# Kernel tuning notes

Measured on AMD Instinct MI355X. Metric: run time of the kernel, lower is better.

Reference implementation:

```python
import jax, jax.numpy as jnp
import numpy as np

H = 2048        # hidden_size
NH = 16         # num q heads
NKV = 4         # num kv heads
HD = 128        # head_dim
G = NH // NKV   # GQA group size
B = 32          # batch (decode sequences)
S = 4096        # max kv cache length per sequence
SCALE = HD ** -0.5
NEG = -1e30


def setup_inputs() -> dict:
    key = jax.random.key(0)
    ks = jax.random.split(key, 6)
    hidden_states = jax.random.normal(ks[0], (B, 1, H), dtype=jnp.float32)
    kv_cache = jax.random.normal(ks[1], (B, S, 2, NKV, HD), dtype=jnp.float32)
    seq_lens = jax.random.randint(ks[2], (B,), 1, S, dtype=jnp.int32)
    slot_mapping = seq_lens - 1  # write current token's k/v at its slot
    positions = (seq_lens - 1)[:, None].astype(jnp.int32)
    Wqkv = jax.random.normal(ks[3], (H, (NH + 2 * NKV) * HD), dtype=jnp.float32) * (H ** -0.5)
    bqkv = jax.random.normal(ks[4], ((NH + 2 * NKV) * HD,), dtype=jnp.float32) * 0.02
    Wo = jax.random.normal(ks[5], (NH * HD, H), dtype=jnp.float32) * ((NH * HD) ** -0.5)
    return {"hidden_states": hidden_states, "positions": positions, "kv_cache": kv_cache,
            "slot_mapping": slot_mapping, "seq_lens": seq_lens,
            "Wqkv": Wqkv, "bqkv": bqkv, "Wo": Wo}


def reference(hidden_states, positions, kv_cache, slot_mapping, seq_lens, Wqkv, bqkv, Wo):
    b, t, _ = hidden_states.shape  # t == 1 (decode)
    qkv = hidden_states.reshape(b * t, H) @ Wqkv + bqkv          # [B, (NH+2NKV)*HD]
    q, k, v = jnp.split(qkv, [NH * HD, (NH + NKV) * HD], axis=-1)
    q = q.reshape(b, NKV, G, HD)                                  # grouped-query layout
    k = k.reshape(b, NKV, HD)
    v = v.reshape(b, NKV, HD)
    # scatter current-step k/v into the paged cache at slot_mapping
    rows = jnp.arange(b)
    cache = kv_cache.at[rows, slot_mapping, 0].set(k)
    cache = cache.at[rows, slot_mapping, 1].set(v)
    keys = cache[:, :, 0]   # [B, S, NKV, HD]
    vals = cache[:, :, 1]   # [B, S, NKV, HD]
    # attention scores with ragged seq_lens mask
    scores = jnp.einsum('bkgd,bskd->bkgs', q, keys) * SCALE       # [B, NKV, G, S]
    valid = (jnp.arange(S)[None, :] < seq_lens[:, None])          # [B, S]
    scores = jnp.where(valid[:, None, None, :], scores, NEG)
    probs = jax.nn.softmax(scores, axis=-1)
    out = jnp.einsum('bkgs,bskd->bkgd', probs, vals)              # [B, NKV, G, HD]
    out = out.reshape(b * t, NH * HD)
    return (out @ Wo).reshape(b, t, H)
```

## Files before the change

kernel.cpp:

```cpp
#include <hip/hip_runtime.h>
#include <cstddef>

#define HQ 2048
#define NKVH 4
#define HDIM 128
#define QKV_N 3072
#define ATT_SCALE 0.08838834764831845f
#define KSPLIT 16
#define CHUNK 128
#define NCH 32

__device__ __forceinline__ float4 f4max(float4 a, float4 b) {
  return make_float4(fmaxf(a.x, b.x), fmaxf(a.y, b.y), fmaxf(a.z, b.z), fmaxf(a.w, b.w));
}

template <int N>
__global__ __launch_bounds__(256) void proj_kernel(const float* __restrict__ X,
                                                   const float* __restrict__ W,
                                                   float* __restrict__ part) {
  __shared__ union {
    float x[32][128];
    float red[32][4][64];
  } sm;
  const int t = threadIdx.x;
  const int c0 = blockIdx.x << 6;
  const int ksb = blockIdx.y;
  const int k0 = ksb << 7;
  const int c = t & 63;
  const int ksub = t >> 6;

#pragma unroll
  for (int i = 0; i < 4; ++i) {
    const int id = t + (i << 8);
    const int bb = id >> 5, kk = (id & 31) << 2;
    *reinterpret_cast<float4*>(&sm.x[bb][kk]) =
        *reinterpret_cast<const float4*>(X + bb * HQ + k0 + kk);
  }
  __syncthreads();

  float acc[32];
#pragma unroll
  for (int b = 0; b < 32; ++b) acc[b] = 0.f;

#pragma unroll
  for (int kk4 = 0; kk4 < 8; ++kk4) {
    const int kk = (ksub << 5) + (kk4 << 2);
    const float* wp = W + (size_t)(k0 + kk) * N + c0 + c;
    const float w0 = wp[0];
    const float w1 = wp[N];
    const float w2 = wp[2 * N];
    const float w3 = wp[3 * N];
#pragma unroll
    for (int b = 0; b < 32; ++b) {
      const float4 x4 = *reinterpret_cast<const float4*>(&sm.x[b][kk]);
      acc[b] = fmaf(x4.x, w0, acc[b]);
      acc[b] = fmaf(x4.y, w1, acc[b]);
      acc[b] = fmaf(x4.z, w2, acc[b]);
      acc[b] = fmaf(x4.w, w3, acc[b]);
    }
  }
  __syncthreads();
#pragma unroll
  for (int b = 0; b < 32; ++b) sm.red[b][ksub][c] = acc[b];
  __syncthreads();
#pragma unroll
  for (int i = 0; i < 8; ++i) {
    const int o = t + (i << 8);
    const int b = o >> 6, cc = o & 63;
    const float v = sm.red[b][0][cc] + sm.red[b][1][cc] + sm.red[b][2][cc] + sm.red[b][3][cc];
    part[(size_t)(ksb * 32 + b) * N + c0 + cc] = v;
  }
}

template <int NCOL, bool HAS_BIAS>
__global__ __launch_bounds__(256) void reduce_kernel(const float* __restrict__ part,
                                                     const float* __restrict__ bias,
                                                     float* __restrict__ out) {
  const int o = blockIdx.x * 256 + threadIdx.x;
  constexpr int total = 32 * NCOL;
  float s = 0.f;
#pragma unroll
  for (int ks = 0; ks < KSPLIT; ++ks) s += part[(size_t)ks * total + o];
  if (HAS_BIAS) s += bias[o % NCOL];
  out[o] = s;
}

__global__ __launch_bounds__(256) void attn_kernel(const float* __restrict__ cache,
                                                   const int* __restrict__ seq_lens,
                                                   const int* __restrict__ slot_map,
                                                   const float* __restrict__ qkv,
                                                   float* __restrict__ ml,
                                                   float* __restrict__ accp) {
  __shared__ float pt[CHUNK][4];
  __shared__ float pvbuf[4][128][4];
  __shared__ float redm[4][4];
  __shared__ float redl[4][4];

  const int t = threadIdx.x;
  const int bid = blockIdx.x;
  const int chunk = bid & 31;
  const int kvh = (bid >> 5) & 3;
  const int b = bid >> 7;
  const int L = seq_lens[b];
  const int start = chunk << 7;
  if (start >= L) return;
  const int n = min(CHUNK, L - start);
  const int send = start + n;
  const int slot = slot_map[b];
  const float* __restrict__ qrow = qkv + b * QKV_N;
  const float* __restrict__ knew = qrow + 2048 + (kvh << 7);
  const float* __restrict__ vnew = qrow + 2560 + (kvh << 7);

  const int w = t >> 6, l = t & 63;
  const int l16 = l & 15, rq = l >> 4;
  const int wbase = w << 5;

  float4 qr[4][2];
#pragma unroll
  for (int g = 0; g < 4; ++g) {
#pragma unroll
    for (int e = 0; e < 2; ++e)
      qr[g][e] = *reinterpret_cast<const float4*>(qrow + ((kvh << 2) + g) * HDIM +
                                                  (l16 << 3) + (e << 2));
  }

  auto krow_ptr = [&](int r) -> const float* {
    int sg = start + r;
    sg = (sg < send) ? sg : start;
    return (sg == slot) ? knew : cache + (((size_t)((b << 12) + sg)) << 10) + (kvh << 7);
  };
  auto vrow_ptr = [&](int r) -> const float* {
    int sg = start + r;
    sg = (sg < send) ? sg : start;
    return (sg == slot) ? vnew : cache + (((size_t)((b << 12) + sg)) << 10) + 512 + (kvh << 7);
  };

  auto kload = [&](int st, float4* dst) {
#pragma unroll
    for (int rg = 0; rg < 4; ++rg) {
      const float* kp = krow_ptr(wbase + (st << 4) + (rg << 2) + rq) + (l16 << 3);
      dst[2 * rg] = *reinterpret_cast<const float4*>(kp);
      dst[2 * rg + 1] = *reinterpret_cast<const float4*>(kp + 4);
    }
  };
  auto vload = [&](int vt, float2* dst) {
#pragma unroll
    for (int s = 0; s < 16; ++s)
      dst[s] = *reinterpret_cast<const float2*>(vrow_ptr(wbase + (vt << 4) + s) + (l << 1));
  };

  float4 m4 = make_float4(-1e30f, -1e30f, -1e30f, -1e30f);
  auto score_st = [&](int st, const float4* kr) {
#pragma unroll
    for (int rg = 0; rg < 4; ++rg) {
      const float4 k0 = kr[2 * rg], k1 = kr[2 * rg + 1];
      float s0 = fmaf(k0.x, qr[0][0].x, fmaf(k0.y, qr[0][0].y, fmaf(k0.z, qr[0][0].z, k0.w * qr[0][0].w)));
      s0 = fmaf(k1.x, qr[0][1].x, fmaf(k1.y, qr[0][1].y, fmaf(k1.z, qr[0][1].z, fmaf(k1.w, qr[0][1].w, s0))));
      float s1 = fmaf(k0.x, qr[1][0].x, fmaf(k0.y, qr[1][0].y, fmaf(k0.z, qr[1][0].z, k0.w * qr[1][0].w)));
      s1 = fmaf(k1.x, qr[1][1].x, fmaf(k1.y, qr[1][1].y, fmaf(k1.z, qr[1][1].z, fmaf(k1.w, qr[1][1].w, s1))));
      float s2 = fmaf(k0.x, qr[2][0].x, fmaf(k0.y, qr[2][0].y, fmaf(k0.z, qr[2][0].z, k0.w * qr[2][0].w)));
      s2 = fmaf(k1.x, qr[2][1].x, fmaf(k1.y, qr[2][1].y, fmaf(k1.z, qr[2][1].z, fmaf(k1.w, qr[2][1].w, s2))));
      float s3 = fmaf(k0.x, qr[3][0].x, fmaf(k0.y, qr[3][0].y, fmaf(k0.z, qr[3][0].z, k0.w * qr[3][0].w)));
      s3 = fmaf(k1.x, qr[3][1].x, fmaf(k1.y, qr[3][1].y, fmaf(k1.z, qr[3][1].z, fmaf(k1.w, qr[3][1].w, s3))));
#pragma unroll
      for (int off = 1; off <= 8; off <<= 1) {
        s0 += __shfl_xor(s0, off);
        s1 += __shfl_xor(s1, off);
        s2 += __shfl_xor(s2, off);
        s3 += __shfl_xor(s3, off);
      }
      const int row = wbase + (st << 4) + (rg << 2) + rq;
      const float4 sc = make_float4(s0 * ATT_SCALE, s1 * ATT_SCALE, s2 * ATT_SCALE, s3 * ATT_SCALE);
      if (row < n) m4 = f4max(m4, sc);
      if (l16 == 0) *reinterpret_cast<float4*>(&pt[row][0]) = sc;
    }
  };

  float4 ka[8];
  float2 va[16], vb[16];
  kload(0, ka);
  vload(0, va);
  score_st(0, ka);
  kload(1, ka);
  score_st(1, ka);

  m4.x = fmaxf(m4.x, __shfl_xor(m4.x, 16));
  m4.y = fmaxf(m4.y, __shfl_xor(m4.y, 16));
  m4.z = fmaxf(m4.z, __shfl_xor(m4.z, 16));
  m4.w = fmaxf(m4.w, __shfl_xor(m4.w, 16));
  m4.x = fmaxf(m4.x, __shfl_xor(m4.x, 32));
  m4.y = fmaxf(m4.y, __shfl_xor(m4.y, 32));
  m4.z = fmaxf(m4.z, __shfl_xor(m4.z, 32));
  m4.w = fmaxf(m4.w, __shfl_xor(m4.w, 32));
  if (l == 0) *reinterpret_cast<float4*>(&redm[w][0]) = m4;
  __syncthreads();
  float4 M4 = *reinterpret_cast<const float4*>(&redm[0][0]);
  M4 = f4max(M4, *reinterpret_cast<const float4*>(&redm[1][0]));
  M4 = f4max(M4, *reinterpret_cast<const float4*>(&redm[2][0]));
  M4 = f4max(M4, *reinterpret_cast<const float4*>(&redm[3][0]));

  vload(1, vb);

  float4 l4 = make_float4(0.f, 0.f, 0.f, 0.f);
  if (l < 32) {
    const int r = wbase + l;
    float4 e = make_float4(0.f, 0.f, 0.f, 0.f);
    if (r < n) {
      const float4 v = *reinterpret_cast<const float4*>(&pt[r][0]);
      e.x = __expf(v.x - M4.x);
      e.y = __expf(v.y - M4.y);
      e.z = __expf(v.z - M4.z);
      e.w = __expf(v.w - M4.w);
    }
    *reinterpret_cast<float4*>(&pt[r][0]) = e;
    l4 = e;
  }
#pragma unroll
  for (int off = 1; off <= 32; off <<= 1) {
    l4.x += __shfl_xor(l4.x, off);
    l4.y += __shfl_xor(l4.y, off);
    l4.z += __shfl_xor(l4.z, off);
    l4.w += __shfl_xor(l4.w, off);
  }
  if (l == 0) *reinterpret_cast<float4*>(&redl[w][0]) = l4;

  float4 accA = make_float4(0.f, 0.f, 0.f, 0.f);
  float4 accB = make_float4(0.f, 0.f, 0.f, 0.f);
#pragma unroll
  for (int s = 0; s < 16; ++s) {
    const float4 p = *reinterpret_cast<const float4*>(&pt[wbase + s][0]);
    const float2 vv = va[s];
    accA.x = fmaf(p.x, vv.x, accA.x); accA.y = fmaf(p.y, vv.x, accA.y);
    accA.z = fmaf(p.z, vv.x, accA.z); accA.w = fmaf(p.w, vv.x, accA.w);
    accB.x = fmaf(p.x, vv.y, accB.x); accB.y = fmaf(p.y, vv.y, accB.y);
    accB.z = fmaf(p.z, vv.y, accB.z); accB.w = fmaf(p.w, vv.y, accB.w);
  }
#pragma unroll
  for (int s = 0; s < 16; ++s) {
    const float4 p = *reinterpret_cast<const float4*>(&pt[wbase + 16 + s][0]);
    const float2 vv = vb[s];
    accA.x = fmaf(p.x, vv.x, accA.x); accA.y = fmaf(p.y, vv.x, accA.y);
    accA.z = fmaf(p.z, vv.x, accA.z); accA.w = fmaf(p.w, vv.x, accA.w);
    accB.x = fmaf(p.x, vv.y, accB.x); accB.y = fmaf(p.y, vv.y, accB.y);
    accB.z = fmaf(p.z, vv.y, accB.z); accB.w = fmaf(p.w, vv.y, accB.w);
  }

  *reinterpret_cast<float4*>(&pvbuf[w][l << 1][0]) = accA;
  *reinterpret_cast<float4*>(&pvbuf[w][(l << 1) + 1][0]) = accB;
  __syncthreads();

  if (t < 128) {
    const int d = t;
    float4 s0 = *reinterpret_cast<const float4*>(&pvbuf[0][d][0]);
    const float4 s1 = *reinterpret_cast<const float4*>(&pvbuf[1][d][0]);
    const float4 s2 = *reinterpret_cast<const float4*>(&pvbuf[2][d][0]);
    const float4 s3 = *reinterpret_cast<const float4*>(&pvbuf[3][d][0]);
    s0.x += s1.x + s2.x + s3.x;
    s0.y += s1.y + s2.y + s3.y;
    s0.z += s1.z + s2.z + s3.z;
    s0.w += s1.w + s2.w + s3.w;
    float* ap = accp + (size_t)bid * 512;
    ap[d] = s0.x;
    ap[128 + d] = s0.y;
    ap[256 + d] = s0.z;
    ap[384 + d] = s0.w;
  }
  if (t == 0) {
    float4 Lt = *reinterpret_cast<const float4*>(&redl[0][0]);
    const float4 l1 = *reinterpret_cast<const float4*>(&redl[1][0]);
    const float4 l2 = *reinterpret_cast<const float4*>(&redl[2][0]);
    const float4 l3 = *reinterpret_cast<const float4*>(&redl[3][0]);
    Lt.x += l1.x + l2.x + l3.x;
    Lt.y += l1.y + l2.y + l3.y;
    Lt.z += l1.z + l2.z + l3.z;
    Lt.w += l1.w + l2.w + l3.w;
    *reinterpret_cast<float4*>(ml + (size_t)bid * 8) = M4;
    *reinterpret_cast<float4*>(ml + (size_t)bid * 8 + 4) = Lt;
  }
}

__global__ __launch_bounds__(128) void combine_kernel(const int* __restrict__ seq_lens,
                                                      const float* __restrict__ ml,
                                                      const float* __restrict__ accp,
                                                      float* __restrict__ attn) {
  const int blk = blockIdx.x;
  const int g = blk & 3, kvh = (blk >> 2) & 3, b = blk >> 4;
  const int d = threadIdx.x;
  const int L = seq_lens[b];
  const int nch = (L + CHUNK - 1) >> 7;
  const int base = (b * 4 + kvh) * NCH;

  float M = -1e30f;
  for (int c = 0; c < nch; ++c) M = fmaxf(M, ml[(size_t)(base + c) * 8 + g]);
  float osum = 0.f, lsum = 0.f;
  for (int c = 0; c < nch; ++c) {
    const int idx = base + c;
    const float mc = ml[(size_t)idx * 8 + g];
    const float lc = ml[(size_t)idx * 8 + 4 + g];
    const float wgt = __expf(mc - M);
    lsum = fmaf(lc, wgt, lsum);
    osum = fmaf(wgt, accp[(size_t)idx * 512 + g * 128 + d], osum);
  }
  attn[(size_t)b * HQ + kvh * 512 + g * 128 + d] = osum / lsum;
}

extern "C" void kernel_launch(void* const* d_in, const int* in_sizes, int n_in,
                              void* d_out, int out_size, void* d_ws, size_t ws_size,
                              hipStream_t stream) {
  const float* hidden = (const float*)d_in[0];
  const float* cache = (const float*)d_in[2];
  const int* slot_map = (const int*)d_in[3];
  const int* seq_lens = (const int*)d_in[4];
  const float* Wqkv = (const float*)d_in[5];
  const float* bqkv = (const float*)d_in[6];
  const float* Wo = (const float*)d_in[7];
  float* out = (float*)d_out;
  float* ws = (float*)d_ws;

  float* qkv_part = ws;
  float* qkv      = ws + 1572864;
  float* ml       = ws + 1671168;
  float* accp     = ws + 1703936;
  float* attn     = ws + 3801088;
  float* o_part   = ws + 3866624;

  proj_kernel<QKV_N><<<dim3(48, KSPLIT), 256, 0, stream>>>(hidden, Wqkv, qkv_part);
  reduce_kernel<QKV_N, true><<<384, 256, 0, stream>>>(qkv_part, bqkv, qkv);
  attn_kernel<<<4096, 256, 0, stream>>>(cache, seq_lens, slot_map, qkv, ml, accp);
  combine_kernel<<<512, 128, 0, stream>>>(seq_lens, ml, accp, attn);
  proj_kernel<HQ><<<dim3(32, KSPLIT), 256, 0, stream>>>(attn, Wo, o_part);
  reduce_kernel<HQ, false><<<256, 256, 0, stream>>>(o_part, nullptr, out);
}
```

Measured before the change: 125.0 us.

## Halve attention chunk size to 64 rows and keep scores in registers

Split the KV sequence into 64-row chunks instead of 128, doubling the attention grid so more blocks can keep memory requests in flight. Each wave now handles 16 rows, so scores stay in registers and the softmax exponentials are computed in place, which removes the shared-memory round trip for raw scores. A launch-bounds occupancy hint is added. The cost is more partial results for the combine kernel to read and more per-block overhead for short sequences.

```diff
diff --git a/kernel.cpp b/kernel.cpp
--- a/kernel.cpp
+++ b/kernel.cpp
@@ -7,8 +7,8 @@
 #define QKV_N 3072
 #define ATT_SCALE 0.08838834764831845f
 #define KSPLIT 16
-#define CHUNK 128
-#define NCH 32
+#define CHUNK 64
+#define NCH 64
 
 __device__ __forceinline__ float4 f4max(float4 a, float4 b) {
   return make_float4(fmaxf(a.x, b.x), fmaxf(a.y, b.y), fmaxf(a.z, b.z), fmaxf(a.w, b.w));
@@ -85,24 +85,24 @@
   out[o] = s;
 }
 
-__global__ __launch_bounds__(256) void attn_kernel(const float* __restrict__ cache,
-                                                   const int* __restrict__ seq_lens,
-                                                   const int* __restrict__ slot_map,
-                                                   const float* __restrict__ qkv,
-                                                   float* __restrict__ ml,
-                                                   float* __restrict__ accp) {
-  __shared__ float pt[CHUNK][4];
+__global__ __launch_bounds__(256, 4) void attn_kernel(const float* __restrict__ cache,
+                                                      const int* __restrict__ seq_lens,
+                                                      const int* __restrict__ slot_map,
+                                                      const float* __restrict__ qkv,
+                                                      float* __restrict__ ml,
+                                                      float* __restrict__ accp) {
+  __shared__ float pt[4][16][4];
   __shared__ float pvbuf[4][128][4];
   __shared__ float redm[4][4];
   __shared__ float redl[4][4];
 
   const int t = threadIdx.x;
   const int bid = blockIdx.x;
-  const int chunk = bid & 31;
-  const int kvh = (bid >> 5) & 3;
-  const int b = bid >> 7;
+  const int chunk = bid & 63;
+  const int kvh = (bid >> 6) & 3;
+  const int b = bid >> 8;
   const int L = seq_lens[b];
-  const int start = chunk << 7;
+  const int start = chunk << 6;
   if (start >= L) return;
   const int n = min(CHUNK, L - start);
   const int send = start + n;
@@ -113,16 +113,7 @@
 
   const int w = t >> 6, l = t & 63;
   const int l16 = l & 15, rq = l >> 4;
-  const int wbase = w << 5;
-
-  float4 qr[4][2];
-#pragma unroll
-  for (int g = 0; g < 4; ++g) {
-#pragma unroll
-    for (int e = 0; e < 2; ++e)
-      qr[g][e] = *reinterpret_cast<const float4*>(qrow + ((kvh << 2) + g) * HDIM +
-                                                  (l16 << 3) + (e << 2));
-  }
+  const int wbase = w << 4;
 
   auto krow_ptr = [&](int r) -> const float* {
     int sg = start + r;
@@ -135,54 +126,49 @@
     return (sg == slot) ? vnew : cache + (((size_t)((b << 12) + sg)) << 10) + 512 + (kvh << 7);
   };
 
-  auto kload = [&](int st, float4* dst) {
-#pragma unroll
-    for (int rg = 0; rg < 4; ++rg) {
-      const float* kp = krow_ptr(wbase + (st << 4) + (rg << 2) + rq) + (l16 << 3);
-      dst[2 * rg] = *reinterpret_cast<const float4*>(kp);
-      dst[2 * rg + 1] = *reinterpret_cast<const float4*>(kp + 4);
+  float4 qr[4][2];
+#pragma unroll
+  for (int g = 0; g < 4; ++g) {
+#pragma unroll
+    for (int e = 0; e < 2; ++e)
+      qr[g][e] = *reinterpret_cast<const float4*>(qrow + ((kvh << 2) + g) * HDIM +
+                                                  (l16 << 3) + (e << 2));
+  }
+  float4 ka[8];
+#pragma unroll
+  for (int rg = 0; rg < 4; ++rg) {
+    const float* kp = krow_ptr(wbase + (rg << 2) + rq) + (l16 << 3);
+    ka[2 * rg] = *reinterpret_cast<const float4*>(kp);
+    ka[2 * rg + 1] = *reinterpret_cast<const float4*>(kp + 4);
+  }
+  float2 va[16];
+#pragma unroll
+  for (int s = 0; s < 16; ++s)
+    va[s] = *reinterpret_cast<const float2*>(vrow_ptr(wbase + s) + (l << 1));
+
+  float4 m4 = make_float4(-1e30f, -1e30f, -1e30f, -1e30f);
+  float4 scr[4];
+#pragma unroll
+  for (int rg = 0; rg < 4; ++rg) {
+    const float4 k0 = ka[2 * rg], k1 = ka[2 * rg + 1];
+    float s0 = fmaf(k0.x, qr[0][0].x, fmaf(k0.y, qr[0][0].y, fmaf(k0.z, qr[0][0].z, k0.w * qr[0][0].w)));
+    s0 = fmaf(k1.x, qr[0][1].x, fmaf(k1.y, qr[0][1].y, fmaf(k1.z, qr[0][1].z, fmaf(k1.w, qr[0][1].w, s0))));
+    float s1 = fmaf(k0.x, qr[1][0].x, fmaf(k0.y, qr[1][0].y, fmaf(k0.z, qr[1][0].z, k0.w * qr[1][0].w)));
+    s1 = fmaf(k1.x, qr[1][1].x, fmaf(k1.y, qr[1][1].y, fmaf(k1.z, qr[1][1].z, fmaf(k1.w, qr[1][1].w, s1))));
+    float s2 = fmaf(k0.x, qr[2][0].x, fmaf(k0.y, qr[2][0].y, fmaf(k0.z, qr[2][0].z, k0.w * qr[2][0].w)));
+    s2 = fmaf(k1.x, qr[2][1].x, fmaf(k1.y, qr[2][1].y, fmaf(k1.z, qr[2][1].z, fmaf(k1.w, qr[2][1].w, s2))));
+    float s3 = fmaf(k0.x, qr[3][0].x, fmaf(k0.y, qr[3][0].y, fmaf(k0.z, qr[3][0].z, k0.w * qr[3][0].w)));
+    s3 = fmaf(k1.x, qr[3][1].x, fmaf(k1.y, qr[3][1].y, fmaf(k1.z, qr[3][1].z, fmaf(k1.w, qr[3][1].w, s3))));
+#pragma unroll
+    for (int off = 1; off <= 8; off <<= 1) {
+      s0 += __shfl_xor(s0, off);
+      s1 += __shfl_xor(s1, off);
+      s2 += __shfl_xor(s2, off);
+      s3 += __shfl_xor(s3, off);
     }
-  };
-  auto vload = [&](int vt, float2* dst) {
-#pragma unroll
-    for (int s = 0; s < 16; ++s)
-      dst[s] = *reinterpret_cast<const float2*>(vrow_ptr(wbase + (vt << 4) + s) + (l << 1));
-  };
-
-  float4 m4 = make_float4(-1e30f, -1e30f, -1e30f, -1e30f);
-  auto score_st = [&](int st, const float4* kr) {
-#pragma unroll
-    for (int rg = 0; rg < 4; ++rg) {
-      const float4 k0 = kr[2 * rg], k1 = kr[2 * rg + 1];
-      float s0 = fmaf(k0.x, qr[0][0].x, fmaf(k0.y, qr[0][0].y, fmaf(k0.z, qr[0][0].z, k0.w * qr[0][0].w)));
-      s0 = fmaf(k1.x, qr[0][1].x, fmaf(k1.y, qr[0][1].y, fmaf(k1.z, qr[0][1].z, fmaf(k1.w, qr[0][1].w, s0))));
-      float s1 = fmaf(k0.x, qr[1][0].x, fmaf(k0.y, qr[1][0].y, fmaf(k0.z, qr[1][0].z, k0.w * qr[1][0].w)));
-      s1 = fmaf(k1.x, qr[1][1].x, fmaf(k1.y, qr[1][1].y, fmaf(k1.z, qr[1][1].z, fmaf(k1.w, qr[1][1].w, s1))));
-      float s2 = fmaf(k0.x, qr[2][0].x, fmaf(k0.y, qr[2][0].y, fmaf(k0.z, qr[2][0].z, k0.w * qr[2][0].w)));
-      s2 = fmaf(k1.x, qr[2][1].x, fmaf(k1.y, qr[2][1].y, fmaf(k1.z, qr[2][1].z, fmaf(k1.w, qr[2][1].w, s2))));
-      float s3 = fmaf(k0.x, qr[3][0].x, fmaf(k0.y, qr[3][0].y, fmaf(k0.z, qr[3][0].z, k0.w * qr[3][0].w)));
-      s3 = fmaf(k1.x, qr[3][1].x, fmaf(k1.y, qr[3][1].y, fmaf(k1.z, qr[3][1].z, fmaf(k1.w, qr[3][1].w, s3))));
-#pragma unroll
-      for (int off = 1; off <= 8; off <<= 1) {
-        s0 += __shfl_xor(s0, off);
-        s1 += __shfl_xor(s1, off);
-        s2 += __shfl_xor(s2, off);
-        s3 += __shfl_xor(s3, off);
-      }
-      const int row = wbase + (st << 4) + (rg << 2) + rq;
-      const float4 sc = make_float4(s0 * ATT_SCALE, s1 * ATT_SCALE, s2 * ATT_SCALE, s3 * ATT_SCALE);
-      if (row < n) m4 = f4max(m4, sc);
-      if (l16 == 0) *reinterpret_cast<float4*>(&pt[row][0]) = sc;
-    }
-  };
-
-  float4 ka[8];
-  float2 va[16], vb[16];
-  kload(0, ka);
-  vload(0, va);
-  score_st(0, ka);
-  kload(1, ka);
-  score_st(1, ka);
+    scr[rg] = make_float4(s0 * ATT_SCALE, s1 * ATT_SCALE, s2 * ATT_SCALE, s3 * ATT_SCALE);
+    if (wbase + (rg << 2) + rq < n) m4 = f4max(m4, scr[rg]);
+  }
 
   m4.x = fmaxf(m4.x, __shfl_xor(m4.x, 16));
   m4.y = fmaxf(m4.y, __shfl_xor(m4.y, 16));
@@ -199,46 +185,33 @@
   M4 = f4max(M4, *reinterpret_cast<const float4*>(&redm[2][0]));
   M4 = f4max(M4, *reinterpret_cast<const float4*>(&redm[3][0]));
 
-  vload(1, vb);
-
-  float4 l4 = make_float4(0.f, 0.f, 0.f, 0.f);
-  if (l < 32) {
-    const int r = wbase + l;
+  float4 lsum = make_float4(0.f, 0.f, 0.f, 0.f);
+#pragma unroll
+  for (int rg = 0; rg < 4; ++rg) {
+    const int row = wbase + (rg << 2) + rq;
     float4 e = make_float4(0.f, 0.f, 0.f, 0.f);
-    if (r < n) {
-      const float4 v = *reinterpret_cast<const float4*>(&pt[r][0]);
-      e.x = __expf(v.x - M4.x);
-      e.y = __expf(v.y - M4.y);
-      e.z = __expf(v.z - M4.z);
-      e.w = __expf(v.w - M4.w);
+    if (row < n) {
+      e.x = __expf(scr[rg].x - M4.x);
+      e.y = __expf(scr[rg].y - M4.y);
+      e.z = __expf(scr[rg].z - M4.z);
+      e.w = __expf(scr[rg].w - M4.w);
     }
-    *reinterpret_cast<float4*>(&pt[r][0]) = e;
-    l4 = e;
-  }
-#pragma unroll
-  for (int off = 1; off <= 32; off <<= 1) {
-    l4.x += __shfl_xor(l4.x, off);
-    l4.y += __shfl_xor(l4.y, off);
-    l4.z += __shfl_xor(l4.z, off);
-    l4.w += __shfl_xor(l4.w, off);
-  }
-  if (l == 0) *reinterpret_cast<float4*>(&redl[w][0]) = l4;
+    lsum.x += e.x; lsum.y += e.y; lsum.z += e.z; lsum.w += e.w;
+    if (l16 == 0) *reinterpret_cast<float4*>(&pt[w][(rg << 2) + rq][0]) = e;
+  }
+  lsum.x += __shfl_xor(lsum.x, 16); lsum.y += __shfl_xor(lsum.y, 16);
+  lsum.z += __shfl_xor(lsum.z, 16); lsum.w += __shfl_xor(lsum.w, 16);
+  lsum.x += __shfl_xor(lsum.x, 32); lsum.y += __shfl_xor(lsum.y, 32);
+  lsum.z += __shfl_xor(lsum.z, 32); lsum.w += __shfl_xor(lsum.w, 32);
+  if (l == 0) *reinterpret_cast<float4*>(&redl[w][0]) = lsum;
+  asm volatile("s_waitcnt lgkmcnt(0)" ::: "memory");
 
   float4 accA = make_float4(0.f, 0.f, 0.f, 0.f);
   float4 accB = make_float4(0.f, 0.f, 0.f, 0.f);
 #pragma unroll
   for (int s = 0; s < 16; ++s) {
-    const float4 p = *reinterpret_cast<const float4*>(&pt[wbase + s][0]);
+    const float4 p = *reinterpret_cast<const float4*>(&pt[w][s][0]);
     const float2 vv = va[s];
-    accA.x = fmaf(p.x, vv.x, accA.x); accA.y = fmaf(p.y, vv.x, accA.y);
-    accA.z = fmaf(p.z, vv.x, accA.z); accA.w = fmaf(p.w, vv.x, accA.w);
-    accB.x = fmaf(p.x, vv.y, accB.x); accB.y = fmaf(p.y, vv.y, accB.y);
-    accB.z = fmaf(p.z, vv.y, accB.z); accB.w = fmaf(p.w, vv.y, accB.w);
-  }
-#pragma unroll
-  for (int s = 0; s < 16; ++s) {
-    const float4 p = *reinterpret_cast<const float4*>(&pt[wbase + 16 + s][0]);
-    const float2 vv = vb[s];
     accA.x = fmaf(p.x, vv.x, accA.x); accA.y = fmaf(p.y, vv.x, accA.y);
     accA.z = fmaf(p.z, vv.x, accA.z); accA.w = fmaf(p.w, vv.x, accA.w);
     accB.x = fmaf(p.x, vv.y, accB.x); accB.y = fmaf(p.y, vv.y, accB.y);
@@ -287,7 +260,7 @@
   const int g = blk & 3, kvh = (blk >> 2) & 3, b = blk >> 4;
   const int d = threadIdx.x;
   const int L = seq_lens[b];
-  const int nch = (L + CHUNK - 1) >> 7;
+  const int nch = (L + CHUNK - 1) >> 6;
   const int base = (b * 4 + kvh) * NCH;
 
   float M = -1e30f;
@@ -320,13 +293,13 @@
   float* qkv_part = ws;
   float* qkv      = ws + 1572864;
   float* ml       = ws + 1671168;
-  float* accp     = ws + 1703936;
-  float* attn     = ws + 3801088;
-  float* o_part   = ws + 3866624;
+  float* accp     = ws + 1736704;
+  float* attn     = ws + 5931008;
+  float* o_part   = ws + 5996544;
 
   proj_kernel<QKV_N><<<dim3(48, KSPLIT), 256, 0, stream>>>(hidden, Wqkv, qkv_part);
   reduce_kernel<QKV_N, true><<<384, 256, 0, stream>>>(qkv_part, bqkv, qkv);
-  attn_kernel<<<4096, 256, 0, stream>>>(cache, seq_lens, slot_map, qkv, ml, accp);
+  attn_kernel<<<8192, 256, 0, stream>>>(cache, seq_lens, slot_map, qkv, ml, accp);
   combine_kernel<<<512, 128, 0, stream>>>(seq_lens, ml, accp, attn);
   proj_kernel<HQ><<<dim3(32, KSPLIT), 256, 0, stream>>>(attn, Wo, o_part);
   reduce_kernel<HQ, false><<<256, 256, 0, stream>>>(o_part, nullptr, out);
```

New measurement: 132.6 us. 6.1% more time.
